# Optimization experiments

Measured on AMD Instinct MI355X. Metric: run time of the kernel, lower is better.

## Reference

```python
import jax, jax.numpy as jnp
import numpy as np

TOKEN_DIM = 1024
HIDDEN = 256
NUM_FREQS = 10
FOURIER_DIM = 3 * (2 * NUM_FREQS + 1)  # include_input + sin/cos per freq = 63
EPS_LN = 1e-5
EPS_NORM = 1e-12


def fourier_encode(x):
    # x: [..., 3] -> [..., 3*(1+2*NUM_FREQS)]
    freqs = (2.0 ** jnp.arange(NUM_FREQS)).astype(x.dtype)  # [F]
    xf = x[..., None] * freqs  # [..., 3, F]
    sin = jnp.sin(xf)
    cos = jnp.cos(xf)
    enc = jnp.concatenate([x[..., None], sin, cos], axis=-1)  # [..., 3, 1+2F]
    return enc.reshape(*x.shape[:-1], FOURIER_DIM)


def layer_norm(x, g, b):
    mu = jnp.mean(x, axis=-1, keepdims=True)
    var = jnp.mean((x - mu) ** 2, axis=-1, keepdims=True)
    return (x - mu) * jax.lax.rsqrt(var + EPS_LN) * g + b


def setup_inputs() -> dict:
    key = jax.random.key(0)
    ks = jax.random.split(key, 12)
    B, T, N = 2, 512, 40000
    in_dim = TOKEN_DIM + FOURIER_DIM
    s1 = 1.0 / np.sqrt(in_dim)
    s2 = 1.0 / np.sqrt(HIDDEN)
    return {
        "transformer_tokens": jax.random.normal(ks[0], (B, T, TOKEN_DIM), jnp.float32),
        "scaffold_anchors": jax.random.normal(ks[1], (B, T, 3), jnp.float32),
        "scaffold_token_ids": jax.random.randint(ks[2], (B, N), 0, T, jnp.int32),
        "W1": jax.random.uniform(ks[3], (in_dim, HIDDEN), jnp.float32, -s1, s1),
        "b1": jnp.zeros((HIDDEN,), jnp.float32),
        "g1": jnp.ones((HIDDEN,), jnp.float32),
        "be1": jnp.zeros((HIDDEN,), jnp.float32),
        "W2": jax.random.uniform(ks[4], (HIDDEN, HIDDEN), jnp.float32, -s2, s2),
        "b2": jnp.zeros((HIDDEN,), jnp.float32),
        "g2": jnp.ones((HIDDEN,), jnp.float32),
        "be2": jnp.zeros((HIDDEN,), jnp.float32),
        "W3": jax.random.uniform(ks[5], (HIDDEN, 14), jnp.float32, -s2, s2),
        "b3": jnp.zeros((14,), jnp.float32),
    }


def reference(transformer_tokens, scaffold_anchors, scaffold_token_ids,
              W1, b1, g1, be1, W2, b2, g2, be2, W3, b3):
    B, T, D = transformer_tokens.shape
    N = scaffold_token_ids.shape[1]
    idx = scaffold_token_ids.astype(jnp.int32)
    # Gather per-Gaussian anchors and token features: [B, N, 3] / [B, N, D]
    per_anchor = jnp.take_along_axis(scaffold_anchors, idx[..., None], axis=1)
    token_feats = jnp.take_along_axis(transformer_tokens, idx[..., None], axis=1)
    spatial_enc = fourier_encode(per_anchor)  # [B, N, FOURIER_DIM]
    combined = jnp.concatenate([token_feats, spatial_enc], axis=-1)
    h = jax.nn.relu(layer_norm(combined @ W1 + b1, g1, be1))
    h = jax.nn.relu(layer_norm(h @ W2 + b2, g2, be2))
    raw = h @ W3 + b3  # [B, N, 14]
    pos = raw[..., 0:3]
    color = jnp.clip(raw[..., 3:6], 0.0, 1.0)
    opac = jax.nn.sigmoid(raw[..., 6:7])
    scale = jnp.exp(raw[..., 7:10])
    q = raw[..., 10:14]
    qn = jnp.linalg.norm(q, axis=-1, keepdims=True)
    quat = q / jnp.maximum(qn, EPS_NORM)
    out = jnp.concatenate([pos, color, opac, scale, quat], axis=-1)
    return out.reshape(B, N * 14)
```

## Files before the change

kernel.cpp:

```cpp
#include <hip/hip_runtime.h>

#define TDIM   1024
#define HID    256
#define FDIM   63
#define INDIM  1087
#define TT     512
#define NBATCH 2
#define ROWS   4
#define KC     64
#define EPS_LN   1e-5f
#define EPS_NORM 1e-12f

__device__ __forceinline__ float wave_reduce_sum(float v) {
    #pragma unroll
    for (int m = 32; m >= 1; m >>= 1) v += __shfl_xor(v, m);
    return v;
}

__global__ __launch_bounds__(256) void stage1_kernel(
    const float* __restrict__ tokens,
    const float* __restrict__ anchors,
    const float* __restrict__ W1,
    const float* __restrict__ b1,
    float* __restrict__ h1_pre)
{
    __shared__ float comb_lds[16][KC];
    __shared__ float fr_lds[16][64];

    const int tid     = threadIdx.x;
    const int rt      = blockIdx.x >> 2;
    const int cg      = blockIdx.x & 3;
    const int rowbase = rt * 16;
    const int col     = (cg << 6) + (tid & 63);
    const int rg4     = (tid >> 6) << 2;

    for (int u0 = tid; u0 < 16 * FDIM; u0 += 256) {
        const int r = u0 / FDIM;
        const int u = u0 % FDIM;
        const int c = u / 21;
        const int w = u % 21;
        const float x = anchors[(size_t)(rowbase + r) * 3 + c];
        float v;
        if (w == 0)       v = x;
        else if (w <= 10) v = sinf(x * (float)(1u << (w - 1)));
        else              v = cosf(x * (float)(1u << (w - 11)));
        fr_lds[r][u] = v;
    }

    float acc0 = b1[col];
    float acc1 = acc0, acc2 = acc0, acc3 = acc0;

    const int sr = tid >> 4;
    const int sj = (tid & 15) << 2;

    float4 pf = *(const float4*)&tokens[(size_t)(rowbase + sr) * TDIM + sj];
    __syncthreads();

    for (int c = 0; c < 16; ++c) {
        *(float4*)&comb_lds[sr][sj] = pf;
        __syncthreads();
        if (c < 15)
            pf = *(const float4*)&tokens[(size_t)(rowbase + sr) * TDIM + (c + 1) * KC + sj];
        const int k0 = c * KC;
        const float* __restrict__ wp = W1 + (size_t)k0 * HID + col;
        #pragma unroll
        for (int kk = 0; kk < KC; kk += 4) {
            const float w0 = wp[(size_t)(kk    ) * HID];
            const float w1 = wp[(size_t)(kk + 1) * HID];
            const float w2 = wp[(size_t)(kk + 2) * HID];
            const float w3 = wp[(size_t)(kk + 3) * HID];
            const float4 c0 = *(const float4*)&comb_lds[rg4 + 0][kk];
            const float4 c1 = *(const float4*)&comb_lds[rg4 + 1][kk];
            const float4 c2 = *(const float4*)&comb_lds[rg4 + 2][kk];
            const float4 c3 = *(const float4*)&comb_lds[rg4 + 3][kk];
            acc0 = fmaf(c0.x, w0, acc0); acc0 = fmaf(c0.y, w1, acc0);
            acc0 = fmaf(c0.z, w2, acc0); acc0 = fmaf(c0.w, w3, acc0);
            acc1 = fmaf(c1.x, w0, acc1); acc1 = fmaf(c1.y, w1, acc1);
            acc1 = fmaf(c1.z, w2, acc1); acc1 = fmaf(c1.w, w3, acc1);
            acc2 = fmaf(c2.x, w0, acc2); acc2 = fmaf(c2.y, w1, acc2);
            acc2 = fmaf(c2.z, w2, acc2); acc2 = fmaf(c2.w, w3, acc2);
            acc3 = fmaf(c3.x, w0, acc3); acc3 = fmaf(c3.y, w1, acc3);
            acc3 = fmaf(c3.z, w2, acc3); acc3 = fmaf(c3.w, w3, acc3);
        }
        __syncthreads();
    }

    const float* __restrict__ wt = W1 + (size_t)TDIM * HID + col;
    for (int kk = 0; kk < FDIM; ++kk) {
        const float w = wt[(size_t)kk * HID];
        acc0 = fmaf(fr_lds[rg4 + 0][kk], w, acc0);
        acc1 = fmaf(fr_lds[rg4 + 1][kk], w, acc1);
        acc2 = fmaf(fr_lds[rg4 + 2][kk], w, acc2);
        acc3 = fmaf(fr_lds[rg4 + 3][kk], w, acc3);
    }

    h1_pre[(size_t)(rowbase + rg4 + 0) * HID + col] = acc0;
    h1_pre[(size_t)(rowbase + rg4 + 1) * HID + col] = acc1;
    h1_pre[(size_t)(rowbase + rg4 + 2) * HID + col] = acc2;
    h1_pre[(size_t)(rowbase + rg4 + 3) * HID + col] = acc3;
}

__global__ __launch_bounds__(256) void decode_tail_kernel(
    const float* __restrict__ h1_pre,
    const float* __restrict__ g1,
    const float* __restrict__ be1,
    const float* __restrict__ W2,
    const float* __restrict__ b2,
    const float* __restrict__ g2,
    const float* __restrict__ be2,
    const float* __restrict__ W3,
    const float* __restrict__ b3,
    float* __restrict__ decoded)
{
    __shared__ float h1[ROWS][HID];
    __shared__ float h2[ROWS][HID];
    __shared__ float raws[ROWS][16];

    const int tid  = threadIdx.x;
    const int base = blockIdx.x * ROWS;
    const int wave = tid >> 6;
    const int lane = tid & 63;

    {
        const int r = wave;
        const float* __restrict__ src = h1_pre + (size_t)(base + r) * HID;
        float x0 = src[lane], x1 = src[lane + 64], x2 = src[lane + 128], x3 = src[lane + 192];
        const float ga0 = g1[lane], ga1 = g1[lane + 64], ga2 = g1[lane + 128], ga3 = g1[lane + 192];
        const float bb0 = be1[lane], bb1 = be1[lane + 64], bb2 = be1[lane + 128], bb3 = be1[lane + 192];
        const float s  = wave_reduce_sum(x0 + x1 + x2 + x3);
        const float mu = s * (1.0f / 256.0f);
        const float d0 = x0 - mu, d1 = x1 - mu, d2 = x2 - mu, d3 = x3 - mu;
        const float sq = wave_reduce_sum(d0 * d0 + d1 * d1 + d2 * d2 + d3 * d3);
        const float rstd = 1.0f / sqrtf(sq * (1.0f / 256.0f) + EPS_LN);
        h1[r][lane]       = fmaxf(0.0f, fmaf(d0 * rstd, ga0, bb0));
        h1[r][lane + 64]  = fmaxf(0.0f, fmaf(d1 * rstd, ga1, bb1));
        h1[r][lane + 128] = fmaxf(0.0f, fmaf(d2 * rstd, ga2, bb2));
        h1[r][lane + 192] = fmaxf(0.0f, fmaf(d3 * rstd, ga3, bb3));
    }
    __syncthreads();

    {
        float acc[ROWS];
        const float bias = b2[tid];
        #pragma unroll
        for (int r = 0; r < ROWS; ++r) acc[r] = bias;
        const float* __restrict__ wp = W2 + tid;
        #pragma unroll 8
        for (int k = 0; k < HID; ++k) {
            const float w = wp[(size_t)k * HID];
            #pragma unroll
            for (int r = 0; r < ROWS; ++r) acc[r] = fmaf(h1[r][k], w, acc[r]);
        }
        #pragma unroll
        for (int r = 0; r < ROWS; ++r) h2[r][tid] = acc[r];
    }
    __syncthreads();

    {
        const float ga0 = g2[lane], ga1 = g2[lane + 64], ga2 = g2[lane + 128], ga3 = g2[lane + 192];
        const float bb0 = be2[lane], bb1 = be2[lane + 64], bb2 = be2[lane + 128], bb3 = be2[lane + 192];
        const int r = wave;
        float x0 = h2[r][lane], x1 = h2[r][lane + 64], x2 = h2[r][lane + 128], x3 = h2[r][lane + 192];
        const float s  = wave_reduce_sum(x0 + x1 + x2 + x3);
        const float mu = s * (1.0f / 256.0f);
        const float d0 = x0 - mu, d1 = x1 - mu, d2 = x2 - mu, d3 = x3 - mu;
        const float sq = wave_reduce_sum(d0 * d0 + d1 * d1 + d2 * d2 + d3 * d3);
        const float rstd = 1.0f / sqrtf(sq * (1.0f / 256.0f) + EPS_LN);
        h2[r][lane]       = fmaxf(0.0f, fmaf(d0 * rstd, ga0, bb0));
        h2[r][lane + 64]  = fmaxf(0.0f, fmaf(d1 * rstd, ga1, bb1));
        h2[r][lane + 128] = fmaxf(0.0f, fmaf(d2 * rstd, ga2, bb2));
        h2[r][lane + 192] = fmaxf(0.0f, fmaf(d3 * rstd, ga3, bb3));
    }
    __syncthreads();

    if (tid < ROWS * 14) {
        const int r = tid / 14;
        const int m = tid % 14;
        float a = b3[m];
        #pragma unroll 4
        for (int k = 0; k < HID; ++k) a = fmaf(h2[r][k], W3[k * 14 + m], a);
        raws[r][m] = a;
    }
    __syncthreads();

    if (tid < ROWS * 14) {
        const int r = tid / 14;
        const int m = tid % 14;
        const float x = raws[r][m];
        float v;
        if (m < 3) {
            v = x;
        } else if (m < 6) {
            v = fminf(fmaxf(x, 0.0f), 1.0f);
        } else if (m == 6) {
            v = 1.0f / (1.0f + expf(-x));
        } else if (m < 10) {
            v = expf(x);
        } else {
            const float q0 = raws[r][10], q1 = raws[r][11];
            const float q2 = raws[r][12], q3 = raws[r][13];
            const float nrm = sqrtf(q0 * q0 + q1 * q1 + q2 * q2 + q3 * q3);
            v = x / fmaxf(nrm, EPS_NORM);
        }
        decoded[(size_t)(base + r) * 14 + m] = v;
    }
}

__global__ __launch_bounds__(256) void gather_kernel(
    const int* __restrict__ ids,
    const float* __restrict__ decoded,
    float* __restrict__ out,
    int N, int total14)
{
    const int j = blockIdx.x * blockDim.x + threadIdx.x;
    if (j >= total14) return;
    const int i = j / 14;
    const int k = j - i * 14;
    const int b = (i >= N) ? 1 : 0;
    const int t = ids[i];
    out[j] = decoded[(size_t)(b * TT + t) * 14 + k];
}

extern "C" void kernel_launch(void* const* d_in, const int* in_sizes, int n_in,
                              void* d_out, int out_size, void* d_ws, size_t ws_size,
                              hipStream_t stream) {
    const float* tokens  = (const float*)d_in[0];
    const float* anchors = (const float*)d_in[1];
    const int*   ids     = (const int*)d_in[2];
    const float* W1  = (const float*)d_in[3];
    const float* b1  = (const float*)d_in[4];
    const float* g1  = (const float*)d_in[5];
    const float* be1 = (const float*)d_in[6];
    const float* W2  = (const float*)d_in[7];
    const float* b2  = (const float*)d_in[8];
    const float* g2  = (const float*)d_in[9];
    const float* be2 = (const float*)d_in[10];
    const float* W3  = (const float*)d_in[11];
    const float* b3  = (const float*)d_in[12];

    const size_t n_h1   = (size_t)1024 * HID;
    const size_t n_dec  = (size_t)1024 * 14;

    float* decoded = (float*)d_ws;
    float* h1_pre;
    if (ws_size >= (n_h1 + n_dec) * sizeof(float)) {
        h1_pre = (float*)d_ws + n_dec;
    } else {
        h1_pre = (float*)d_out;
    }
    float* out = (float*)d_out;

    const int N = in_sizes[2] / NBATCH;

    stage1_kernel<<<256, 256, 0, stream>>>(tokens, anchors, W1, b1, h1_pre);

    decode_tail_kernel<<<1024 / ROWS, 256, 0, stream>>>(
        h1_pre, g1, be1, W2, b2, g2, be2, W3, b3, decoded);

    const int total14 = NBATCH * N * 14;
    gather_kernel<<<(total14 + 255) / 256, 256, 0, stream>>>(ids, decoded, out, N, total14);
}
```

Measured before the change: 150.1 us.

## Split-K first layer into partial sums, reduce partials in decode tail

Replaces the LDS-tiled first GEMM with a split-K kernel: each 512-thread block covers 16 rows and one quarter of the 1087-long K dimension, and each thread accumulates float4 column outputs for two rows. Tokens are read straight from global memory, and Fourier features are computed inline in the tail chunk. The four partial buffers, stored in the output buffer, are summed together with b1 in the decode tail. The W2 matmul is also rewritten so that each wave handles one row with float4 weight loads. The aim is more parallelism and vectorized weight loads, at the cost of extra partial-sum traffic and redundant per-wave W2 reads.

```diff
diff --git a/kernel.cpp b/kernel.cpp
--- a/kernel.cpp
+++ b/kernel.cpp
@@ -6,10 +6,17 @@
 #define INDIM  1087
 #define TT     512
 #define NBATCH 2
-#define ROWS   4
-#define KC     64
+#define NROWS  1024
+#define KSPLIT 4
+#define KCHUNK 272
 #define EPS_LN   1e-5f
 #define EPS_NORM 1e-12f
+
+#define FMA4(A, s, W)                                   \
+    (A).x = fmaf((s), (W).x, (A).x);                    \
+    (A).y = fmaf((s), (W).y, (A).y);                    \
+    (A).z = fmaf((s), (W).z, (A).z);                    \
+    (A).w = fmaf((s), (W).w, (A).w)
 
 __device__ __forceinline__ float wave_reduce_sum(float v) {
     #pragma unroll
@@ -17,91 +24,83 @@
     return v;
 }
 
-__global__ __launch_bounds__(256) void stage1_kernel(
+__device__ __forceinline__ float fourier_val(const float* __restrict__ anchors, int row, int u) {
+    const int c = u / 21;
+    const int w = u % 21;
+    const float x = anchors[row * 3 + c];
+    if (w == 0)  return x;
+    if (w <= 10) return sinf(x * (float)(1u << (w - 1)));
+    return cosf(x * (float)(1u << (w - 11)));
+}
+
+__global__ __launch_bounds__(512) void stage1_partial_kernel(
     const float* __restrict__ tokens,
     const float* __restrict__ anchors,
     const float* __restrict__ W1,
+    float* __restrict__ part)
+{
+    const int tid    = threadIdx.x;
+    const int rt     = blockIdx.x >> 2;
+    const int z      = blockIdx.x & 3;
+    const int kstart = z * KCHUNK;
+    const int kcount = min(KCHUNK, INDIM - kstart);
+    const int wave   = tid >> 6;
+    const int c4     = (tid & 63) << 2;
+    const int row0   = rt * 16 + wave * 2;
+
+    const float* __restrict__ t0p = tokens + (size_t)(row0 + 0) * TDIM;
+    const float* __restrict__ t1p = tokens + (size_t)(row0 + 1) * TDIM;
+
+    float4 acc0 = {0.f, 0.f, 0.f, 0.f};
+    float4 acc1 = acc0;
+
+    const int glim = kcount >> 2;
+    const int gtok = (kstart < TDIM) ? min(glim, (TDIM - kstart) >> 2) : 0;
+
+    #pragma unroll 4
+    for (int g = 0; g < gtok; ++g) {
+        const int k = kstart + (g << 2);
+        const float4 w0 = *(const float4*)&W1[(size_t)(k + 0) * HID + c4];
+        const float4 w1 = *(const float4*)&W1[(size_t)(k + 1) * HID + c4];
+        const float4 w2 = *(const float4*)&W1[(size_t)(k + 2) * HID + c4];
+        const float4 w3 = *(const float4*)&W1[(size_t)(k + 3) * HID + c4];
+        const float4 s0 = *(const float4*)&t0p[k];
+        const float4 s1 = *(const float4*)&t1p[k];
+        FMA4(acc0, s0.x, w0); FMA4(acc0, s0.y, w1); FMA4(acc0, s0.z, w2); FMA4(acc0, s0.w, w3);
+        FMA4(acc1, s1.x, w0); FMA4(acc1, s1.y, w1); FMA4(acc1, s1.z, w2); FMA4(acc1, s1.w, w3);
+    }
+
+    for (int g = gtok; g < glim; ++g) {
+        const int k = kstart + (g << 2);
+        const float4 w0 = *(const float4*)&W1[(size_t)(k + 0) * HID + c4];
+        const float4 w1 = *(const float4*)&W1[(size_t)(k + 1) * HID + c4];
+        const float4 w2 = *(const float4*)&W1[(size_t)(k + 2) * HID + c4];
+        const float4 w3 = *(const float4*)&W1[(size_t)(k + 3) * HID + c4];
+        const int u = k - TDIM;
+        float4 s0, s1;
+        s0.x = fourier_val(anchors, row0 + 0, u);     s0.y = fourier_val(anchors, row0 + 0, u + 1);
+        s0.z = fourier_val(anchors, row0 + 0, u + 2); s0.w = fourier_val(anchors, row0 + 0, u + 3);
+        s1.x = fourier_val(anchors, row0 + 1, u);     s1.y = fourier_val(anchors, row0 + 1, u + 1);
+        s1.z = fourier_val(anchors, row0 + 1, u + 2); s1.w = fourier_val(anchors, row0 + 1, u + 3);
+        FMA4(acc0, s0.x, w0); FMA4(acc0, s0.y, w1); FMA4(acc0, s0.z, w2); FMA4(acc0, s0.w, w3);
+        FMA4(acc1, s1.x, w0); FMA4(acc1, s1.y, w1); FMA4(acc1, s1.z, w2); FMA4(acc1, s1.w, w3);
+    }
+
+    for (int k = kstart + (glim << 2); k < kstart + kcount; ++k) {
+        const float4 w = *(const float4*)&W1[(size_t)k * HID + c4];
+        const float v0 = (k < TDIM) ? t0p[k] : fourier_val(anchors, row0 + 0, k - TDIM);
+        const float v1 = (k < TDIM) ? t1p[k] : fourier_val(anchors, row0 + 1, k - TDIM);
+        FMA4(acc0, v0, w); FMA4(acc1, v1, w);
+    }
+
+    float* __restrict__ pb = part + (size_t)z * NROWS * HID;
+    *(float4*)&pb[(size_t)(row0 + 0) * HID + c4] = acc0;
+    *(float4*)&pb[(size_t)(row0 + 1) * HID + c4] = acc1;
+}
+
+__global__ __launch_bounds__(256) void decode_tail_kernel(
+    const float* __restrict__ part,
     const float* __restrict__ b1,
-    float* __restrict__ h1_pre)
-{
-    __shared__ float comb_lds[16][KC];
-    __shared__ float fr_lds[16][64];
-
-    const int tid     = threadIdx.x;
-    const int rt      = blockIdx.x >> 2;
-    const int cg      = blockIdx.x & 3;
-    const int rowbase = rt * 16;
-    const int col     = (cg << 6) + (tid & 63);
-    const int rg4     = (tid >> 6) << 2;
-
-    for (int u0 = tid; u0 < 16 * FDIM; u0 += 256) {
-        const int r = u0 / FDIM;
-        const int u = u0 % FDIM;
-        const int c = u / 21;
-        const int w = u % 21;
-        const float x = anchors[(size_t)(rowbase + r) * 3 + c];
-        float v;
-        if (w == 0)       v = x;
-        else if (w <= 10) v = sinf(x * (float)(1u << (w - 1)));
-        else              v = cosf(x * (float)(1u << (w - 11)));
-        fr_lds[r][u] = v;
-    }
-
-    float acc0 = b1[col];
-    float acc1 = acc0, acc2 = acc0, acc3 = acc0;
-
-    const int sr = tid >> 4;
-    const int sj = (tid & 15) << 2;
-
-    float4 pf = *(const float4*)&tokens[(size_t)(rowbase + sr) * TDIM + sj];
-    __syncthreads();
-
-    for (int c = 0; c < 16; ++c) {
-        *(float4*)&comb_lds[sr][sj] = pf;
-        __syncthreads();
-        if (c < 15)
-            pf = *(const float4*)&tokens[(size_t)(rowbase + sr) * TDIM + (c + 1) * KC + sj];
-        const int k0 = c * KC;
-        const float* __restrict__ wp = W1 + (size_t)k0 * HID + col;
-        #pragma unroll
-        for (int kk = 0; kk < KC; kk += 4) {
-            const float w0 = wp[(size_t)(kk    ) * HID];
-            const float w1 = wp[(size_t)(kk + 1) * HID];
-            const float w2 = wp[(size_t)(kk + 2) * HID];
-            const float w3 = wp[(size_t)(kk + 3) * HID];
-            const float4 c0 = *(const float4*)&comb_lds[rg4 + 0][kk];
-            const float4 c1 = *(const float4*)&comb_lds[rg4 + 1][kk];
-            const float4 c2 = *(const float4*)&comb_lds[rg4 + 2][kk];
-            const float4 c3 = *(const float4*)&comb_lds[rg4 + 3][kk];
-            acc0 = fmaf(c0.x, w0, acc0); acc0 = fmaf(c0.y, w1, acc0);
-            acc0 = fmaf(c0.z, w2, acc0); acc0 = fmaf(c0.w, w3, acc0);
-            acc1 = fmaf(c1.x, w0, acc1); acc1 = fmaf(c1.y, w1, acc1);
-            acc1 = fmaf(c1.z, w2, acc1); acc1 = fmaf(c1.w, w3, acc1);
-            acc2 = fmaf(c2.x, w0, acc2); acc2 = fmaf(c2.y, w1, acc2);
-            acc2 = fmaf(c2.z, w2, acc2); acc2 = fmaf(c2.w, w3, acc2);
-            acc3 = fmaf(c3.x, w0, acc3); acc3 = fmaf(c3.y, w1, acc3);
-            acc3 = fmaf(c3.z, w2, acc3); acc3 = fmaf(c3.w, w3, acc3);
-        }
-        __syncthreads();
-    }
-
-    const float* __restrict__ wt = W1 + (size_t)TDIM * HID + col;
-    for (int kk = 0; kk < FDIM; ++kk) {
-        const float w = wt[(size_t)kk * HID];
-        acc0 = fmaf(fr_lds[rg4 + 0][kk], w, acc0);
-        acc1 = fmaf(fr_lds[rg4 + 1][kk], w, acc1);
-        acc2 = fmaf(fr_lds[rg4 + 2][kk], w, acc2);
-        acc3 = fmaf(fr_lds[rg4 + 3][kk], w, acc3);
-    }
-
-    h1_pre[(size_t)(rowbase + rg4 + 0) * HID + col] = acc0;
-    h1_pre[(size_t)(rowbase + rg4 + 1) * HID + col] = acc1;
-    h1_pre[(size_t)(rowbase + rg4 + 2) * HID + col] = acc2;
-    h1_pre[(size_t)(rowbase + rg4 + 3) * HID + col] = acc3;
-}
-
-__global__ __launch_bounds__(256) void decode_tail_kernel(
-    const float* __restrict__ h1_pre,
     const float* __restrict__ g1,
     const float* __restrict__ be1,
     const float* __restrict__ W2,
@@ -112,19 +111,23 @@
     const float* __restrict__ b3,
     float* __restrict__ decoded)
 {
-    __shared__ float h1[ROWS][HID];
-    __shared__ float h2[ROWS][HID];
-    __shared__ float raws[ROWS][16];
+    __shared__ float h1[4][HID];
+    __shared__ float h2[4][HID];
+    __shared__ float raws[4][16];
 
     const int tid  = threadIdx.x;
-    const int base = blockIdx.x * ROWS;
     const int wave = tid >> 6;
     const int lane = tid & 63;
+    const int row  = blockIdx.x * 4 + wave;
 
     {
-        const int r = wave;
-        const float* __restrict__ src = h1_pre + (size_t)(base + r) * HID;
-        float x0 = src[lane], x1 = src[lane + 64], x2 = src[lane + 128], x3 = src[lane + 192];
+        const size_t off = (size_t)row * HID;
+        float x0 = b1[lane], x1 = b1[lane + 64], x2 = b1[lane + 128], x3 = b1[lane + 192];
+        #pragma unroll
+        for (int zz = 0; zz < KSPLIT; ++zz) {
+            const float* __restrict__ p = part + (size_t)zz * NROWS * HID + off;
+            x0 += p[lane]; x1 += p[lane + 64]; x2 += p[lane + 128]; x3 += p[lane + 192];
+        }
         const float ga0 = g1[lane], ga1 = g1[lane + 64], ga2 = g1[lane + 128], ga3 = g1[lane + 192];
         const float bb0 = be1[lane], bb1 = be1[lane + 64], bb2 = be1[lane + 128], bb3 = be1[lane + 192];
         const float s  = wave_reduce_sum(x0 + x1 + x2 + x3);
@@ -132,48 +135,46 @@
         const float d0 = x0 - mu, d1 = x1 - mu, d2 = x2 - mu, d3 = x3 - mu;
         const float sq = wave_reduce_sum(d0 * d0 + d1 * d1 + d2 * d2 + d3 * d3);
         const float rstd = 1.0f / sqrtf(sq * (1.0f / 256.0f) + EPS_LN);
-        h1[r][lane]       = fmaxf(0.0f, fmaf(d0 * rstd, ga0, bb0));
-        h1[r][lane + 64]  = fmaxf(0.0f, fmaf(d1 * rstd, ga1, bb1));
-        h1[r][lane + 128] = fmaxf(0.0f, fmaf(d2 * rstd, ga2, bb2));
-        h1[r][lane + 192] = fmaxf(0.0f, fmaf(d3 * rstd, ga3, bb3));
+        h1[wave][lane]       = fmaxf(0.0f, fmaf(d0 * rstd, ga0, bb0));
+        h1[wave][lane + 64]  = fmaxf(0.0f, fmaf(d1 * rstd, ga1, bb1));
+        h1[wave][lane + 128] = fmaxf(0.0f, fmaf(d2 * rstd, ga2, bb2));
+        h1[wave][lane + 192] = fmaxf(0.0f, fmaf(d3 * rstd, ga3, bb3));
     }
     __syncthreads();
 
     {
-        float acc[ROWS];
-        const float bias = b2[tid];
-        #pragma unroll
-        for (int r = 0; r < ROWS; ++r) acc[r] = bias;
-        const float* __restrict__ wp = W2 + tid;
-        #pragma unroll 8
-        for (int k = 0; k < HID; ++k) {
-            const float w = wp[(size_t)k * HID];
-            #pragma unroll
-            for (int r = 0; r < ROWS; ++r) acc[r] = fmaf(h1[r][k], w, acc[r]);
+        const int cc = lane << 2;
+        float4 acc = *(const float4*)&b2[cc];
+        #pragma unroll 4
+        for (int k = 0; k < HID; k += 4) {
+            const float4 hk = *(const float4*)&h1[wave][k];
+            const float4 w0 = *(const float4*)&W2[(size_t)(k + 0) * HID + cc];
+            const float4 w1 = *(const float4*)&W2[(size_t)(k + 1) * HID + cc];
+            const float4 w2 = *(const float4*)&W2[(size_t)(k + 2) * HID + cc];
+            const float4 w3 = *(const float4*)&W2[(size_t)(k + 3) * HID + cc];
+            FMA4(acc, hk.x, w0); FMA4(acc, hk.y, w1); FMA4(acc, hk.z, w2); FMA4(acc, hk.w, w3);
         }
-        #pragma unroll
-        for (int r = 0; r < ROWS; ++r) h2[r][tid] = acc[r];
+        *(float4*)&h2[wave][cc] = acc;
     }
     __syncthreads();
 
     {
+        float x0 = h2[wave][lane], x1 = h2[wave][lane + 64], x2 = h2[wave][lane + 128], x3 = h2[wave][lane + 192];
         const float ga0 = g2[lane], ga1 = g2[lane + 64], ga2 = g2[lane + 128], ga3 = g2[lane + 192];
         const float bb0 = be2[lane], bb1 = be2[lane + 64], bb2 = be2[lane + 128], bb3 = be2[lane + 192];
-        const int r = wave;
-        float x0 = h2[r][lane], x1 = h2[r][lane + 64], x2 = h2[r][lane + 128], x3 = h2[r][lane + 192];
         const float s  = wave_reduce_sum(x0 + x1 + x2 + x3);
         const float mu = s * (1.0f / 256.0f);
         const float d0 = x0 - mu, d1 = x1 - mu, d2 = x2 - mu, d3 = x3 - mu;
         const float sq = wave_reduce_sum(d0 * d0 + d1 * d1 + d2 * d2 + d3 * d3);
         const float rstd = 1.0f / sqrtf(sq * (1.0f / 256.0f) + EPS_LN);
-        h2[r][lane]       = fmaxf(0.0f, fmaf(d0 * rstd, ga0, bb0));
-        h2[r][lane + 64]  = fmaxf(0.0f, fmaf(d1 * rstd, ga1, bb1));
-        h2[r][lane + 128] = fmaxf(0.0f, fmaf(d2 * rstd, ga2, bb2));
-        h2[r][lane + 192] = fmaxf(0.0f, fmaf(d3 * rstd, ga3, bb3));
-    }
-    __syncthreads();
-
-    if (tid < ROWS * 14) {
+        h2[wave][lane]       = fmaxf(0.0f, fmaf(d0 * rstd, ga0, bb0));
+        h2[wave][lane + 64]  = fmaxf(0.0f, fmaf(d1 * rstd, ga1, bb1));
+        h2[wave][lane + 128] = fmaxf(0.0f, fmaf(d2 * rstd, ga2, bb2));
+        h2[wave][lane + 192] = fmaxf(0.0f, fmaf(d3 * rstd, ga3, bb3));
+    }
+    __syncthreads();
+
+    if (tid < 4 * 14) {
         const int r = tid / 14;
         const int m = tid % 14;
         float a = b3[m];
@@ -183,7 +184,7 @@
     }
     __syncthreads();
 
-    if (tid < ROWS * 14) {
+    if (tid < 4 * 14) {
         const int r = tid / 14;
         const int m = tid % 14;
         const float x = raws[r][m];
@@ -202,7 +203,7 @@
             const float nrm = sqrtf(q0 * q0 + q1 * q1 + q2 * q2 + q3 * q3);
             v = x / fmaxf(nrm, EPS_NORM);
         }
-        decoded[(size_t)(base + r) * 14 + m] = v;
+        decoded[(size_t)(blockIdx.x * 4 + r) * 14 + m] = v;
     }
 }
 
@@ -238,24 +239,16 @@
     const float* W3  = (const float*)d_in[11];
     const float* b3  = (const float*)d_in[12];
 
-    const size_t n_h1   = (size_t)1024 * HID;
-    const size_t n_dec  = (size_t)1024 * 14;
-
     float* decoded = (float*)d_ws;
-    float* h1_pre;
-    if (ws_size >= (n_h1 + n_dec) * sizeof(float)) {
-        h1_pre = (float*)d_ws + n_dec;
-    } else {
-        h1_pre = (float*)d_out;
-    }
-    float* out = (float*)d_out;
+    float* part    = (float*)d_out;
+    float* out     = (float*)d_out;
 
     const int N = in_sizes[2] / NBATCH;
 
-    stage1_kernel<<<256, 256, 0, stream>>>(tokens, anchors, W1, b1, h1_pre);
-
-    decode_tail_kernel<<<1024 / ROWS, 256, 0, stream>>>(
-        h1_pre, g1, be1, W2, b2, g2, be2, W3, b3, decoded);
+    stage1_partial_kernel<<<64 * KSPLIT, 512, 0, stream>>>(tokens, anchors, W1, part);
+
+    decode_tail_kernel<<<NROWS / 4, 256, 0, stream>>>(
+        part, b1, g1, be1, W2, b2, g2, be2, W3, b3, decoded);
 
     const int total14 = NBATCH * N * 14;
     gather_kernel<<<(total14 + 255) / 256, 256, 0, stream>>>(ids, decoded, out, N, total14);
```

After: 163.6 us. +9.0%, slower.
